# Kernel optimization log

Measured on AMD Instinct MI355X. Metric: run time of the kernel, lower is better.

Reference implementation:

```python
import jax, jax.numpy as jnp
import numpy as np

NUM_CLASSES = 80
NUM_PRIORS = 3
STRIDES = (8, 16, 32)
ANCHORS = (((10, 13), (16, 30), (33, 23)),
           ((30, 61), (62, 45), (59, 119)),
           ((116, 90), (156, 198), (373, 326)))
PRE_TOP_K = 1000
KEEP_TOP_K = 100
IOU_THR = 0.65
SCORE_THR = 0.25
IMG = 640
CLS_OFFSET = 4096.0  # class-offset trick for batched (class-aware) NMS


def _make_priors():
    priors, strides = [], []
    for lvl, s in enumerate(STRIDES):
        fs = IMG // s
        ys, xs = np.meshgrid(np.arange(fs), np.arange(fs), indexing='ij')
        cx = (xs * s).astype(np.float32)[..., None]
        cy = (ys * s).astype(np.float32)[..., None]
        anc = np.asarray(ANCHORS[lvl], np.float32)  # [3,2]
        cx = np.broadcast_to(cx, (fs, fs, NUM_PRIORS))
        cy = np.broadcast_to(cy, (fs, fs, NUM_PRIORS))
        w = np.broadcast_to(anc[None, None, :, 0], (fs, fs, NUM_PRIORS))
        h = np.broadcast_to(anc[None, None, :, 1], (fs, fs, NUM_PRIORS))
        box = np.stack([cx - w / 2, cy - h / 2, cx + w / 2, cy + h / 2], -1).reshape(-1, 4)
        priors.append(box)
        strides.append(np.full((box.shape[0],), s, np.float32))
    return jnp.asarray(np.concatenate(priors)), jnp.asarray(np.concatenate(strides))


def setup_inputs() -> dict:
    key = jax.random.key(0)
    ks = jax.random.split(key, 9)
    shapes = {
        'cls0': (32, 240, 80, 80), 'cls1': (32, 240, 40, 40), 'cls2': (32, 240, 20, 20),
        'bbox0': (32, 12, 80, 80), 'bbox1': (32, 12, 40, 40), 'bbox2': (32, 12, 20, 20),
        'obj0': (32, 3, 80, 80), 'obj1': (32, 3, 40, 40), 'obj2': (32, 3, 20, 20),
    }
    inp = {n: jax.random.normal(k, s, dtype=jnp.float32) for (n, s), k in zip(shapes.items(), ks)}
    priors, strides = _make_priors()
    inp['priors'] = priors
    inp['strides'] = strides
    return inp


def _flatten(x, last):  # [B,C,H,W] -> [B, H*W*priors, last]
    B = x.shape[0]
    return jnp.transpose(x, (0, 2, 3, 1)).reshape(B, -1, last)


def _decode_yolov5(priors, preds, strides):
    # priors [N,4] (x1,y1,x2,y2), preds [B,N,4], strides [N]
    p = jax.nn.sigmoid(preds)
    cx = (priors[:, 0] + priors[:, 2]) * 0.5
    cy = (priors[:, 1] + priors[:, 3]) * 0.5
    w = priors[:, 2] - priors[:, 0]
    h = priors[:, 3] - priors[:, 1]
    xc = (p[..., 0] - 0.5) * 2.0 * strides + cx
    yc = (p[..., 1] - 0.5) * 2.0 * strides + cy
    wp = (p[..., 2] * 2.0) ** 2 * w
    hp = (p[..., 3] * 2.0) ** 2 * h
    return jnp.stack([xc - wp * 0.5, yc - hp * 0.5, xc + wp * 0.5, yc + hp * 0.5], -1)


def _pairwise_iou(b):  # b [K,4]
    area = (b[:, 2] - b[:, 0]) * (b[:, 3] - b[:, 1])
    lt = jnp.maximum(b[:, None, :2], b[None, :, :2])
    rb = jnp.minimum(b[:, None, 2:], b[None, :, 2:])
    wh = jnp.clip(rb - lt, 0.0)
    inter = wh[..., 0] * wh[..., 1]
    return inter / (area[:, None] + area[None, :] - inter + 1e-7)


def _nms_single(boxes, scores):
    # boxes [N,4], scores [N,C]
    flat = scores.reshape(-1)
    top_s, top_i = jax.lax.top_k(flat, PRE_TOP_K)  # sorted desc
    anchor = top_i // NUM_CLASSES
    label = top_i % NUM_CLASSES
    b = boxes[anchor]  # [K,4]
    bo = b + label.astype(boxes.dtype)[:, None] * CLS_OFFSET
    iou = _pairwise_iou(bo)
    valid = top_s > SCORE_THR
    idxs = jnp.arange(PRE_TOP_K)

    def body(i, supp):
        keep_i = jnp.logical_not(supp[i])
        return jnp.where(keep_i & (iou[i] > IOU_THR) & (idxs > i), True, supp)

    supp = jax.lax.fori_loop(0, PRE_TOP_K, body, jnp.logical_not(valid))
    keep = jnp.logical_not(supp) & valid
    k_scores = jnp.where(keep, top_s, 0.0)
    det_s, det_i = jax.lax.top_k(k_scores, KEEP_TOP_K)
    det_b = b[det_i]
    det_l = label[det_i]
    num = jnp.minimum(jnp.sum(keep.astype(jnp.int32)), KEEP_TOP_K)
    return num, det_b, det_s, det_l


def reference(cls0, cls1, cls2, bbox0, bbox1, bbox2, obj0, obj1, obj2, priors, strides):
    cls = jnp.concatenate([_flatten(c, NUM_CLASSES) for c in (cls0, cls1, cls2)], axis=1)
    scores = jax.nn.sigmoid(cls)  # [B,N,C]
    bp = jnp.concatenate([_flatten(b, 4) for b in (bbox0, bbox1, bbox2)], axis=1)
    obj = jnp.concatenate([_flatten(o, 1)[..., 0] for o in (obj0, obj1, obj2)], axis=1)
    scores = scores * jax.nn.sigmoid(obj)[..., None]
    bboxes = _decode_yolov5(priors, bp, strides)  # [B,N,4]
    num, det_b, det_s, det_l = jax.vmap(_nms_single)(bboxes, scores)
    return num, det_b, det_s, det_l
```

## Files before the change

### kernel.cpp

```cpp
#include <hip/hip_runtime.h>
#include <stdint.h>

#define NCLS 80
#define CELLS 8400
#define PRE 1000
#define KEEP 100
#define CAP 4096
#define NBINS 16384
#define NIMG 32
#define SUBS 8
#define SUBCAP 2048
#define GBINS 4096
#define COMPCAP 2048
#define T0 0.75f
#define SCREEN 1.0886f

__device__ __forceinline__ float sigm(float x) { return 1.0f / (1.0f + __expf(-x)); }

__device__ __forceinline__ void lvlinfo(int cell, int& li, int& loc, int& HW) {
  if (cell < 6400)      { li = 0; loc = cell;        HW = 6400; }
  else if (cell < 8000) { li = 1; loc = cell - 6400; HW = 1600; }
  else                  { li = 2; loc = cell - 8000; HW = 400;  }
}

__global__ __launch_bounds__(256) void k_pass1(
    const float* __restrict__ cls0, const float* __restrict__ cls1, const float* __restrict__ cls2,
    const float* __restrict__ obj0, const float* __restrict__ obj1, const float* __restrict__ obj2,
    uint32_t* __restrict__ cnt75, uint64_t* __restrict__ cand75) {
  const int b = blockIdx.y;
  const int bx = blockIdx.x;
  const int sb = bx / 6;
  const int r  = bx - sb * 6;
  const int h  = r & 1;
  const int p  = r >> 1;
  const int c0cell = (sb * 256 + threadIdx.x) * 4;
  if (c0cell >= CELLS) return;
  int li, loc, HW; lvlinfo(c0cell, li, loc, HW);
  const float* cls = li == 0 ? cls0 : (li == 1 ? cls1 : cls2);
  const float* obj = li == 0 ? obj0 : (li == 1 ? obj1 : obj2);

  float4 ov = *(const float4*)(obj + ((size_t)b * 3 + p) * HW + loc);
  float os[4] = { sigm(ov.x), sigm(ov.y), sigm(ov.z), sigm(ov.w) };

  const int sub = bx & (SUBS - 1);
  const float* cp = cls + ((size_t)b * 240 + p * 80 + h * 40) * HW + loc;
  for (int gq = 0; gq < 5; ++gq) {
    float4 v[8];
#pragma unroll
    for (int u = 0; u < 8; ++u)
      v[u] = *(const float4*)(cp + (size_t)(gq * 8 + u) * HW);
#pragma unroll
    for (int u = 0; u < 8; ++u) {
      const int c = h * 40 + gq * 8 + u;
      float vv[4] = { v[u].x, v[u].y, v[u].z, v[u].w };
#pragma unroll
      for (int k = 0; k < 4; ++k) {
        if (vv[k] > SCREEN) {
          float s = sigm(vv[k]) * os[k];
          if (s > T0) {
            uint32_t slot = atomicAdd(&cnt75[b * SUBS + sub], 1u);
            if (slot < SUBCAP) {
              uint32_t flat = (uint32_t)(((c0cell + k) * 3 + p) * 80 + c);
              cand75[((size_t)(b * SUBS + sub)) * SUBCAP + slot] =
                  ((uint64_t)__float_as_uint(s) << 32) | (uint64_t)(0xFFFFFFFFu - flat);
            }
          }
        }
      }
    }
  }
}

__global__ __launch_bounds__(1024) void k_gather(
    const uint64_t* __restrict__ cand75, const uint32_t* __restrict__ cnt75,
    uint32_t* __restrict__ flags,
    const float* __restrict__ bbox0, const float* __restrict__ bbox1, const float* __restrict__ bbox2,
    const float* __restrict__ priors, const float* __restrict__ strides,
    float* __restrict__ topS, int* __restrict__ topLab, float* __restrict__ topBox,
    uint32_t* __restrict__ nvArr) {
  __shared__ uint32_t hist[GBINS];
  __shared__ uint64_t comp[COMPCAP];
  __shared__ uint32_t seg[64];
  __shared__ uint32_t ncomp_s, cb_s;
  const int b = blockIdx.x;
  const int tid = threadIdx.x;
  uint32_t tot = 0; bool bad = false;
  for (int s = 0; s < SUBS; ++s) {
    uint32_t cc = cnt75[b * SUBS + s];
    tot += cc;
    if (cc > SUBCAP) bad = true;
  }
  if (tot < (uint32_t)PRE) bad = true;
  if (bad) { if (tid == 0) flags[b] = 1u; return; }

  for (int i = tid; i < GBINS; i += 1024) hist[i] = 0;
  if (tid == 0) ncomp_s = 0;
  __syncthreads();
  for (int s = 0; s < SUBS; ++s) {
    uint32_t c = cnt75[b * SUBS + s];
    const uint64_t* src = cand75 + ((size_t)(b * SUBS + s)) * SUBCAP;
    for (int i = tid; i < (int)c; i += 1024) {
      uint32_t hi = (uint32_t)(src[i] >> 32);
      uint32_t bin = (hi - 0x3F400000u) >> 10;
      if (bin > GBINS - 1) bin = GBINS - 1;
      atomicAdd(&hist[bin], 1u);
    }
  }
  __syncthreads();
  if (tid < 64) {
    uint32_t s = 0;
    for (int k = 0; k < 64; ++k) s += hist[tid * 64 + k];
    seg[tid] = s;
  }
  __syncthreads();
  if (tid == 0) {
    uint32_t acc = 0; int segi = 0;
    for (int i = 63; i >= 0; --i) {
      if (acc + seg[i] >= (uint32_t)PRE) { segi = i; break; }
      acc += seg[i];
    }
    uint32_t cb = 0;
    for (int k = 63; k >= 0; --k) {
      acc += hist[segi * 64 + k];
      if (acc >= (uint32_t)PRE) { cb = (uint32_t)(segi * 64 + k); break; }
    }
    cb_s = cb;
  }
  __syncthreads();
  const uint32_t cb = cb_s;
  for (int s = 0; s < SUBS; ++s) {
    uint32_t c = cnt75[b * SUBS + s];
    const uint64_t* src = cand75 + ((size_t)(b * SUBS + s)) * SUBCAP;
    for (int i = tid; i < (int)c; i += 1024) {
      uint64_t key = src[i];
      uint32_t hi = (uint32_t)(key >> 32);
      uint32_t bin = (hi - 0x3F400000u) >> 10;
      if (bin > GBINS - 1) bin = GBINS - 1;
      if (bin >= cb) {
        uint32_t pos = atomicAdd(&ncomp_s, 1u);
        if (pos < COMPCAP) comp[pos] = key;
      }
    }
  }
  __syncthreads();
  const uint32_t ncomp = ncomp_s;
  if (ncomp > COMPCAP) { if (tid == 0) flags[b] = 1u; return; }
  const int N = (ncomp <= 1024u) ? 1024 : COMPCAP;
  for (int i = tid; i < N; i += 1024) if (i >= (int)ncomp) comp[i] = 0ull;
  __syncthreads();
  for (int k = 2; k <= N; k <<= 1) {
    for (int j = k >> 1; j > 0; j >>= 1) {
      for (int i = tid; i < N; i += 1024) {
        int p = i ^ j;
        if (p > i) {
          uint64_t a = comp[i], c = comp[p];
          bool asc = (i & k) != 0;
          if (asc ? (a > c) : (a < c)) { comp[i] = c; comp[p] = a; }
        }
      }
      __syncthreads();
    }
  }
  if (tid == 0) nvArr[b] = (uint32_t)PRE;
  for (int t = tid; t < PRE; t += 1024) {
    uint64_t key = comp[t];
    float sc = __uint_as_float((uint32_t)(key >> 32));
    uint32_t flat = 0xFFFFFFFFu - (uint32_t)(key & 0xFFFFFFFFull);
    uint32_t n = flat / 80u; int lab = (int)(flat - n * 80u);
    uint32_t g = n / 3u; uint32_t p = n - g * 3u;
    int li, loc, HW; lvlinfo((int)g, li, loc, HW);
    const float* bb = li == 0 ? bbox0 : (li == 1 ? bbox1 : bbox2);
    size_t o = ((size_t)b * 12 + p * 4) * HW + loc;
    float p0 = sigm(bb[o]);
    float p1 = sigm(bb[o + (size_t)HW]);
    float p2 = sigm(bb[o + 2 * (size_t)HW]);
    float p3 = sigm(bb[o + 3 * (size_t)HW]);
    float4 pr = *(const float4*)(priors + (size_t)n * 4);
    float st = strides[n];
    float cx = (pr.x + pr.z) * 0.5f, cy = (pr.y + pr.w) * 0.5f;
    float w = pr.z - pr.x, hh = pr.w - pr.y;
    float xc = (p0 - 0.5f) * 2.0f * st + cx;
    float yc = (p1 - 0.5f) * 2.0f * st + cy;
    float wp = p2 * 2.0f; wp = wp * wp * w;
    float hp = p3 * 2.0f; hp = hp * hp * hh;
    topS[(size_t)b * PRE + t] = sc;
    topLab[(size_t)b * PRE + t] = lab;
    *(float4*)(topBox + ((size_t)b * PRE + t) * 4) =
        make_float4(xc - wp * 0.5f, yc - hp * 0.5f, xc + wp * 0.5f, yc + hp * 0.5f);
  }
}

__global__ __launch_bounds__(256) void k_zero_hist(uint32_t* __restrict__ hist,
                                                   const uint32_t* __restrict__ flags) {
  __shared__ uint32_t any;
  if (threadIdx.x == 0) {
    uint32_t a = 0;
    for (int i = 0; i < NIMG; ++i) a |= flags[i];
    any = a;
  }
  __syncthreads();
  if (!any) return;
  const int total = NIMG * NBINS;
  for (int i = blockIdx.x * 256 + threadIdx.x; i < total; i += gridDim.x * 256)
    hist[i] = 0;
}

__global__ __launch_bounds__(256) void k_hist_fb(
    const float* __restrict__ cls0, const float* __restrict__ cls1, const float* __restrict__ cls2,
    const float* __restrict__ obj0, const float* __restrict__ obj1, const float* __restrict__ obj2,
    uint32_t* __restrict__ hist, const uint32_t* __restrict__ flags) {
  const int b = blockIdx.y;
  if (flags[b] == 0u) return;
  __shared__ uint32_t h[NBINS];
  for (int i = threadIdx.x; i < NBINS; i += 256) h[i] = 0;
  __syncthreads();
  const int c0 = (blockIdx.x * 256 + threadIdx.x) * 4;
  if (c0 < CELLS) {
    int li, loc, HW; lvlinfo(c0, li, loc, HW);
    const float* cls = li == 0 ? cls0 : (li == 1 ? cls1 : cls2);
    const float* obj = li == 0 ? obj0 : (li == 1 ? obj1 : obj2);
    float os[3][4];
#pragma unroll
    for (int p = 0; p < 3; ++p) {
      float4 o = *(const float4*)(obj + ((size_t)b * 3 + p) * HW + loc);
      os[p][0] = sigm(o.x); os[p][1] = sigm(o.y); os[p][2] = sigm(o.z); os[p][3] = sigm(o.w);
    }
    for (int p = 0; p < 3; ++p) {
      const float* cp = cls + ((size_t)b * 240 + p * 80) * HW + loc;
      for (int c = 0; c < 80; ++c) {
        float4 v = *(const float4*)(cp + (size_t)c * HW);
        float sv[4] = { sigm(v.x) * os[p][0], sigm(v.y) * os[p][1],
                        sigm(v.z) * os[p][2], sigm(v.w) * os[p][3] };
#pragma unroll
        for (int k = 0; k < 4; ++k) {
          if (sv[k] > 0.25f) {
            uint32_t key = (__float_as_uint(sv[k]) - 0x3E800000u) >> 10;
            if (key > NBINS - 1) key = NBINS - 1;
            atomicAdd(&h[key], 1u);
          }
        }
      }
    }
  }
  __syncthreads();
  for (int i = threadIdx.x; i < NBINS; i += 256) {
    uint32_t v = h[i];
    if (v) atomicAdd(&hist[(size_t)b * NBINS + i], v);
  }
}

__global__ __launch_bounds__(256) void k_cutoff_fb(const uint32_t* __restrict__ hist,
                                                   uint32_t* __restrict__ cutoff,
                                                   const uint32_t* __restrict__ flags) {
  const int b = blockIdx.x;
  if (flags[b] == 0u) return;
  __shared__ uint32_t seg[256];
  const uint32_t* hb = hist + (size_t)b * NBINS;
  uint32_t s = 0;
  for (int k = 0; k < 64; ++k) s += hb[threadIdx.x * 64 + k];
  seg[threadIdx.x] = s;
  __syncthreads();
  if (threadIdx.x == 0) {
    uint32_t acc = 0; int segi = -1;
    for (int i = 255; i >= 0; --i) {
      if (acc + seg[i] >= (uint32_t)PRE) { segi = i; break; }
      acc += seg[i];
    }
    uint32_t cut = 0;
    if (segi >= 0) {
      for (int k = 63; k >= 0; --k) {
        acc += hb[segi * 64 + k];
        if (acc >= (uint32_t)PRE) { cut = (uint32_t)(segi * 64 + k); break; }
      }
    }
    cutoff[b] = cut;
  }
}

__global__ __launch_bounds__(256) void k_collect_fb(
    const float* __restrict__ cls0, const float* __restrict__ cls1, const float* __restrict__ cls2,
    const float* __restrict__ obj0, const float* __restrict__ obj1, const float* __restrict__ obj2,
    const uint32_t* __restrict__ cutoff, uint32_t* __restrict__ candCount,
    uint64_t* __restrict__ cand, const uint32_t* __restrict__ flags) {
  const int b = blockIdx.y;
  if (flags[b] == 0u) return;
  const int c0 = (blockIdx.x * 256 + threadIdx.x) * 4;
  if (c0 >= CELLS) return;
  const uint32_t cut = cutoff[b];
  int li, loc, HW; lvlinfo(c0, li, loc, HW);
  const float* cls = li == 0 ? cls0 : (li == 1 ? cls1 : cls2);
  const float* obj = li == 0 ? obj0 : (li == 1 ? obj1 : obj2);
  float os[3][4];
#pragma unroll
  for (int p = 0; p < 3; ++p) {
    float4 o = *(const float4*)(obj + ((size_t)b * 3 + p) * HW + loc);
    os[p][0] = sigm(o.x); os[p][1] = sigm(o.y); os[p][2] = sigm(o.z); os[p][3] = sigm(o.w);
  }
  for (int p = 0; p < 3; ++p) {
    const float* cp = cls + ((size_t)b * 240 + p * 80) * HW + loc;
    for (int c = 0; c < 80; ++c) {
      float4 v = *(const float4*)(cp + (size_t)c * HW);
      float sv[4] = { sigm(v.x) * os[p][0], sigm(v.y) * os[p][1],
                      sigm(v.z) * os[p][2], sigm(v.w) * os[p][3] };
#pragma unroll
      for (int k = 0; k < 4; ++k) {
        float sk = sv[k];
        if (sk > 0.25f) {
          uint32_t key = (__float_as_uint(sk) - 0x3E800000u) >> 10;
          if (key >= cut) {
            uint32_t pos = atomicAdd(&candCount[b], 1u);
            if (pos < CAP) {
              uint32_t flat = (uint32_t)((((c0 + k) * 3 + p) * 80) + c);
              cand[(size_t)b * CAP + pos] =
                  ((uint64_t)__float_as_uint(sk) << 32) | (uint64_t)(0xFFFFFFFFu - flat);
            }
          }
        }
      }
    }
  }
}

__global__ __launch_bounds__(1024) void k_sort_decode_fb(
    const uint64_t* __restrict__ cand, const uint32_t* __restrict__ candCount,
    const float* __restrict__ bbox0, const float* __restrict__ bbox1, const float* __restrict__ bbox2,
    const float* __restrict__ priors, const float* __restrict__ strides,
    float* __restrict__ topS, int* __restrict__ topLab, float* __restrict__ topBox,
    uint32_t* __restrict__ nvArr, const uint32_t* __restrict__ flags) {
  const int b = blockIdx.x;
  if (flags[b] == 0u) return;
  __shared__ uint64_t s[CAP];
  uint32_t cnt = candCount[b]; if (cnt > (uint32_t)CAP) cnt = CAP;
  for (int i = threadIdx.x; i < CAP; i += 1024)
    s[i] = (i < (int)cnt) ? cand[(size_t)b * CAP + i] : 0ull;
  __syncthreads();
  for (int k = 2; k <= CAP; k <<= 1) {
    for (int j = k >> 1; j > 0; j >>= 1) {
      for (int i = threadIdx.x; i < CAP; i += 1024) {
        int p = i ^ j;
        if (p > i) {
          uint64_t a = s[i], c = s[p];
          bool asc = (i & k) != 0;
          if (asc ? (a > c) : (a < c)) { s[i] = c; s[p] = a; }
        }
      }
      __syncthreads();
    }
  }
  const int NV = (int)(cnt < (uint32_t)PRE ? cnt : (uint32_t)PRE);
  if (threadIdx.x == 0) nvArr[b] = (uint32_t)NV;
  for (int t = threadIdx.x; t < PRE; t += 1024) {
    float sc = 0.0f; int lab = 0; float b0 = 0, b1 = 0, b2v = 0, b3 = 0;
    if (t < NV) {
      uint64_t key = s[t];
      sc = __uint_as_float((uint32_t)(key >> 32));
      uint32_t flat = 0xFFFFFFFFu - (uint32_t)(key & 0xFFFFFFFFull);
      uint32_t n = flat / 80u; lab = (int)(flat - n * 80u);
      uint32_t g = n / 3u; uint32_t p = n - g * 3u;
      int li, loc, HW; lvlinfo((int)g, li, loc, HW);
      const float* bb = li == 0 ? bbox0 : (li == 1 ? bbox1 : bbox2);
      size_t o = ((size_t)b * 12 + p * 4) * HW + loc;
      float p0 = sigm(bb[o]);
      float p1 = sigm(bb[o + (size_t)HW]);
      float p2 = sigm(bb[o + 2 * (size_t)HW]);
      float p3 = sigm(bb[o + 3 * (size_t)HW]);
      float4 pr = *(const float4*)(priors + (size_t)n * 4);
      float st = strides[n];
      float cx = (pr.x + pr.z) * 0.5f, cy = (pr.y + pr.w) * 0.5f;
      float w = pr.z - pr.x, hh = pr.w - pr.y;
      float xc = (p0 - 0.5f) * 2.0f * st + cx;
      float yc = (p1 - 0.5f) * 2.0f * st + cy;
      float wp = p2 * 2.0f; wp = wp * wp * w;
      float hp = p3 * 2.0f; hp = hp * hp * hh;
      b0 = xc - wp * 0.5f; b1 = yc - hp * 0.5f; b2v = xc + wp * 0.5f; b3 = yc + hp * 0.5f;
    }
    topS[(size_t)b * PRE + t] = sc;
    topLab[(size_t)b * PRE + t] = lab;
    *(float4*)(topBox + ((size_t)b * PRE + t) * 4) = make_float4(b0, b1, b2v, b3);
  }
}

__global__ __launch_bounds__(256) void k_iou(
    const float* __restrict__ topBox, const int* __restrict__ topLab,
    const uint32_t* __restrict__ nvArr, uint64_t* __restrict__ mask) {
  __shared__ float4 bx[PRE];
  __shared__ int lb[PRE];
  const int b = blockIdx.y;
  const int NV = (int)nvArr[b];
  for (int i = threadIdx.x; i < PRE; i += 256) {
    bx[i] = *(const float4*)(topBox + ((size_t)b * PRE + i) * 4);
    lb[i] = topLab[(size_t)b * PRE + i];
  }
  __syncthreads();
  for (int task = blockIdx.x * 256 + threadIdx.x; task < PRE * 16; task += gridDim.x * 256) {
    const int i = task >> 4, w = task & 15;
    uint64_t m = 0;
    if (i < NV) {
      const float4 a = bx[i]; const int la = lb[i];
      const float areaA = (a.z - a.x) * (a.w - a.y);
      const int j0 = w << 6;
      const int jend = (j0 + 64 < NV) ? j0 + 64 : NV;
      for (int j = (j0 > i + 1 ? j0 : i + 1); j < jend; ++j) {
        if (lb[j] != la) continue;
        const float4 c = bx[j];
        float xx1 = fmaxf(a.x, c.x), yy1 = fmaxf(a.y, c.y);
        float xx2 = fminf(a.z, c.z), yy2 = fminf(a.w, c.w);
        float iw = fmaxf(xx2 - xx1, 0.0f), ih = fmaxf(yy2 - yy1, 0.0f);
        float inter = iw * ih;
        float areaB = (c.z - c.x) * (c.w - c.y);
        float iou = inter / (areaA + areaB - inter + 1e-7f);
        if (iou > 0.65f) m |= (1ull << (j - j0));
      }
    }
    mask[((size_t)b * PRE + i) * 16 + w] = m;
  }
}

__global__ __launch_bounds__(256) void k_scan_out(
    const uint64_t* __restrict__ mask, const float* __restrict__ topS,
    const int* __restrict__ topLab, const float* __restrict__ topBox,
    const uint32_t* __restrict__ nvArr, float* __restrict__ out) {
  __shared__ uint64_t rows[PRE * 16];
  __shared__ uint64_t keepw[16];
  __shared__ uint32_t pref[17];
  const int b = blockIdx.x;
  const int NV = (int)nvArr[b];
  for (int i = threadIdx.x; i < NV * 16; i += 256) rows[i] = mask[(size_t)b * PRE * 16 + i];
  __syncthreads();
  if (threadIdx.x < 64) {
    const int lane = threadIdx.x;
    uint64_t remv = 0, kw = 0;
    for (int w0 = 0; w0 * 64 < NV; ++w0) {
      uint64_t cur = (uint64_t)__shfl((unsigned long long)remv, w0);
      const int ie = (w0 * 64 + 64 < NV) ? w0 * 64 + 64 : NV;
      for (int i = w0 * 64; i < ie; ++i) {
        const int bi = i & 63;
        uint64_t rl = rows[i * 16 + (lane & 15)];
        uint64_t cw = rows[i * 16 + w0];
        const uint64_t keepm = ((cur >> bi) & 1ull) ? 0ull : ~0ull;
        cur |= cw & keepm;
        remv |= rl & keepm;
        kw |= (lane == w0) ? ((1ull << bi) & keepm) : 0ull;
      }
    }
    if (lane < 16) keepw[lane] = kw;
  }
  __syncthreads();
  if (threadIdx.x == 0) {
    uint32_t a = 0;
    for (int w = 0; w < 16; ++w) { pref[w] = a; a += (uint32_t)__popcll((unsigned long long)keepw[w]); }
    pref[16] = a;
  }
  __syncthreads();
  const uint32_t total = pref[16];
  const uint32_t num = total < (uint32_t)KEEP ? total : (uint32_t)KEEP;
  float* o_num = out;
  float* o_box = out + NIMG;
  float* o_s   = out + NIMG + NIMG * KEEP * 4;
  float* o_l   = o_s + NIMG * KEEP;
  if (threadIdx.x == 0) o_num[b] = (float)num;
  const int zstart = NV < KEEP ? NV : KEEP;
  for (int sidx = zstart + threadIdx.x; sidx < KEEP; sidx += 256) {
    ((float4*)o_box)[b * KEEP + sidx] = make_float4(0, 0, 0, 0);
    o_s[b * KEEP + sidx] = 0.0f;
    o_l[b * KEEP + sidx] = 0.0f;
  }
  for (int j = threadIdx.x; j < NV; j += 256) {
    const int wi = j >> 6, bi = j & 63;
    const uint64_t kword = keepw[wi];
    const int isk = (int)((kword >> bi) & 1ull);
    const uint32_t below = pref[wi] + (uint32_t)__popcll((unsigned long long)(kword & ((1ull << bi) - 1ull)));
    const uint32_t slot = isk ? below : (total + (uint32_t)j - below);
    if (slot < (uint32_t)KEEP) {
      ((float4*)o_box)[b * KEEP + slot] = *(const float4*)(topBox + ((size_t)b * PRE + j) * 4);
      o_s[b * KEEP + slot] = isk ? topS[(size_t)b * PRE + j] : 0.0f;
      o_l[b * KEEP + slot] = (float)topLab[(size_t)b * PRE + j];
    }
  }
}

extern "C" void kernel_launch(void* const* d_in, const int* in_sizes, int n_in,
                              void* d_out, int out_size, void* d_ws, size_t ws_size,
                              hipStream_t stream) {
  (void)in_sizes; (void)n_in; (void)out_size; (void)ws_size;
  const float* cls0 = (const float*)d_in[0];
  const float* cls1 = (const float*)d_in[1];
  const float* cls2 = (const float*)d_in[2];
  const float* bbox0 = (const float*)d_in[3];
  const float* bbox1 = (const float*)d_in[4];
  const float* bbox2 = (const float*)d_in[5];
  const float* obj0 = (const float*)d_in[6];
  const float* obj1 = (const float*)d_in[7];
  const float* obj2 = (const float*)d_in[8];
  const float* priors = (const float*)d_in[9];
  const float* strides = (const float*)d_in[10];
  float* out = (float*)d_out;

  char* ws = (char*)d_ws;
  size_t off = 0;
  auto alloc = [&](size_t bytes) -> void* {
    void* p = ws + off;
    off = (off + bytes + 255) & ~(size_t)255;
    return p;
  };
  uint32_t* small     = (uint32_t*)alloc(4096);
  uint32_t* flags     = small;
  uint32_t* cnt75     = small + 32;
  uint32_t* candCount = small + 288;
  uint32_t* cutoff    = small + 320;
  uint32_t* nvArr     = small + 352;
  uint64_t* cand75    = (uint64_t*)alloc((size_t)NIMG * SUBS * SUBCAP * 8);
  uint32_t* hist      = (uint32_t*)alloc((size_t)NIMG * NBINS * 4);
  uint64_t* cand      = (uint64_t*)alloc((size_t)NIMG * CAP * 8);
  float*    topS      = (float*)alloc((size_t)NIMG * PRE * 4);
  int*      topLab    = (int*)alloc((size_t)NIMG * PRE * 4);
  float*    topBox    = (float*)alloc((size_t)NIMG * PRE * 16);
  uint64_t* maskbuf   = (uint64_t*)alloc((size_t)NIMG * PRE * 16 * 8);

  hipMemsetAsync(small, 0, 4096, stream);

  k_pass1<<<dim3(54, NIMG), 256, 0, stream>>>(cls0, cls1, cls2, obj0, obj1, obj2,
                                              cnt75, cand75);
  k_gather<<<NIMG, 1024, 0, stream>>>(cand75, cnt75, flags, bbox0, bbox1, bbox2,
                                      priors, strides, topS, topLab, topBox, nvArr);
  k_zero_hist<<<256, 256, 0, stream>>>(hist, flags);
  dim3 gScan(9, NIMG);
  k_hist_fb<<<gScan, 256, 0, stream>>>(cls0, cls1, cls2, obj0, obj1, obj2, hist, flags);
  k_cutoff_fb<<<NIMG, 256, 0, stream>>>(hist, cutoff, flags);
  k_collect_fb<<<gScan, 256, 0, stream>>>(cls0, cls1, cls2, obj0, obj1, obj2,
                                          cutoff, candCount, cand, flags);
  k_sort_decode_fb<<<NIMG, 1024, 0, stream>>>(cand, candCount, bbox0, bbox1, bbox2,
                                              priors, strides, topS, topLab, topBox, nvArr, flags);
  k_iou<<<dim3(63, NIMG), 256, 0, stream>>>(topBox, topLab, nvArr, maskbuf);
  k_scan_out<<<NIMG, 256, 0, stream>>>(maskbuf, topS, topLab, topBox, nvArr, out);
}
```

Measured before the change: 372.4 us.

## Flatten pass1 into contiguous float4 scan and fuse fallback kernels via last-block

The first pass now walks the class tensor as a flat contiguous float4 stream across many more blocks. It exits early when a block's four vectors are all below the screen threshold and fetches objectness only for surviving values. The fallback path drops the zero-hist, cutoff and sort/decode kernels: histogram zeroing moves into the gather kernel's bail-out path, and cutoff and sort are done by the last-arriving block using atomic counters and fences. This cuts launch count and improves pass1 coalescing and parallelism, but sorting on a 256-thread block is slower and the code relies on fence-based cross-block completion.

```diff
diff --git a/kernel.cpp b/kernel.cpp
--- a/kernel.cpp
+++ b/kernel.cpp
@@ -29,51 +29,61 @@
     uint32_t* __restrict__ cnt75, uint64_t* __restrict__ cand75) {
   const int b = blockIdx.y;
   const int bx = blockIdx.x;
-  const int sb = bx / 6;
-  const int r  = bx - sb * 6;
-  const int h  = r & 1;
-  const int p  = r >> 1;
-  const int c0cell = (sb * 256 + threadIdx.x) * 4;
-  if (c0cell >= CELLS) return;
-  int li, loc, HW; lvlinfo(c0cell, li, loc, HW);
-  const float* cls = li == 0 ? cls0 : (li == 1 ? cls1 : cls2);
-  const float* obj = li == 0 ? obj0 : (li == 1 ? obj1 : obj2);
-
-  float4 ov = *(const float4*)(obj + ((size_t)b * 3 + p) * HW + loc);
-  float os[4] = { sigm(ov.x), sigm(ov.y), sigm(ov.z), sigm(ov.w) };
-
+  int lvl, lb_f4, nf4, HW, cellbase;
+  const float* clsB; const float* objB;
+  if (bx < 375)      { lvl = 0; lb_f4 = bx * 1024;         nf4 = 384000; HW = 6400; cellbase = 0;    clsB = cls0; objB = obj0; }
+  else if (bx < 469) { lvl = 1; lb_f4 = (bx - 375) * 1024; nf4 = 96000;  HW = 1600; cellbase = 6400; clsB = cls1; objB = obj1; }
+  else               { lvl = 2; lb_f4 = (bx - 469) * 1024; nf4 = 24000;  HW = 400;  cellbase = 8000; clsB = cls2; objB = obj2; }
+  const float4* cb4 = (const float4*)(clsB + (size_t)b * 240 * HW);
+  const float* objb = objB + (size_t)b * 3 * HW;
   const int sub = bx & (SUBS - 1);
-  const float* cp = cls + ((size_t)b * 240 + p * 80 + h * 40) * HW + loc;
-  for (int gq = 0; gq < 5; ++gq) {
-    float4 v[8];
+  const int j0 = lb_f4 + threadIdx.x;
+  const int j1 = j0 + 256, j2 = j0 + 512, j3 = j0 + 768;
+
+  float4 v0 = cb4[j0];
+  float4 v1 = cb4[j1 < nf4 ? j1 : j0];
+  float4 v2 = cb4[j2 < nf4 ? j2 : j0];
+  float4 v3 = cb4[j3 < nf4 ? j3 : j0];
+  float m0 = fmaxf(fmaxf(v0.x, v0.y), fmaxf(v0.z, v0.w));
+  float m1 = fmaxf(fmaxf(v1.x, v1.y), fmaxf(v1.z, v1.w));
+  float m2 = fmaxf(fmaxf(v2.x, v2.y), fmaxf(v2.z, v2.w));
+  float m3 = fmaxf(fmaxf(v3.x, v3.y), fmaxf(v3.z, v3.w));
+  if (fmaxf(fmaxf(m0, m1), fmaxf(m2, m3)) <= SCREEN) return;
+
+  auto proc = [&](float4 v, float mv, int j) {
+    if (mv <= SCREEN) return;
+    int ch, w4;
+    if (lvl == 0)      { ch = j / 1600; w4 = j - ch * 1600; }
+    else if (lvl == 1) { ch = j / 400;  w4 = j - ch * 400; }
+    else               { ch = j / 100;  w4 = j - ch * 100; }
+    const int p = ch / 80;
+    const int c = ch - p * 80;
+    float vv[4] = { v.x, v.y, v.z, v.w };
 #pragma unroll
-    for (int u = 0; u < 8; ++u)
-      v[u] = *(const float4*)(cp + (size_t)(gq * 8 + u) * HW);
-#pragma unroll
-    for (int u = 0; u < 8; ++u) {
-      const int c = h * 40 + gq * 8 + u;
-      float vv[4] = { v[u].x, v[u].y, v[u].z, v[u].w };
-#pragma unroll
-      for (int k = 0; k < 4; ++k) {
-        if (vv[k] > SCREEN) {
-          float s = sigm(vv[k]) * os[k];
-          if (s > T0) {
-            uint32_t slot = atomicAdd(&cnt75[b * SUBS + sub], 1u);
-            if (slot < SUBCAP) {
-              uint32_t flat = (uint32_t)(((c0cell + k) * 3 + p) * 80 + c);
-              cand75[((size_t)(b * SUBS + sub)) * SUBCAP + slot] =
-                  ((uint64_t)__float_as_uint(s) << 32) | (uint64_t)(0xFFFFFFFFu - flat);
-            }
+    for (int k = 0; k < 4; ++k) {
+      if (vv[k] > SCREEN) {
+        float ov = objb[p * HW + w4 * 4 + k];
+        float s = sigm(vv[k]) * sigm(ov);
+        if (s > T0) {
+          uint32_t slot = atomicAdd(&cnt75[b * SUBS + sub], 1u);
+          if (slot < SUBCAP) {
+            uint32_t flat = (uint32_t)(((cellbase + w4 * 4 + k) * 3 + p) * 80 + c);
+            cand75[((size_t)(b * SUBS + sub)) * SUBCAP + slot] =
+                ((uint64_t)__float_as_uint(s) << 32) | (uint64_t)(0xFFFFFFFFu - flat);
           }
         }
       }
     }
-  }
+  };
+  proc(v0, m0, j0);
+  if (j1 < nf4) proc(v1, m1, j1);
+  if (j2 < nf4) proc(v2, m2, j2);
+  if (j3 < nf4) proc(v3, m3, j3);
 }
 
 __global__ __launch_bounds__(1024) void k_gather(
     const uint64_t* __restrict__ cand75, const uint32_t* __restrict__ cnt75,
-    uint32_t* __restrict__ flags,
+    uint32_t* __restrict__ flags, uint32_t* __restrict__ histg,
     const float* __restrict__ bbox0, const float* __restrict__ bbox1, const float* __restrict__ bbox2,
     const float* __restrict__ priors, const float* __restrict__ strides,
     float* __restrict__ topS, int* __restrict__ topLab, float* __restrict__ topBox,
@@ -91,7 +101,11 @@
     if (cc > SUBCAP) bad = true;
   }
   if (tot < (uint32_t)PRE) bad = true;
-  if (bad) { if (tid == 0) flags[b] = 1u; return; }
+  if (bad) {
+    if (tid == 0) flags[b] = 1u;
+    for (int i = tid; i < NBINS; i += 1024) histg[(size_t)b * NBINS + i] = 0;
+    return;
+  }
 
   for (int i = tid; i < GBINS; i += 1024) hist[i] = 0;
   if (tid == 0) ncomp_s = 0;
@@ -144,7 +158,11 @@
   }
   __syncthreads();
   const uint32_t ncomp = ncomp_s;
-  if (ncomp > COMPCAP) { if (tid == 0) flags[b] = 1u; return; }
+  if (ncomp > COMPCAP) {
+    if (tid == 0) flags[b] = 1u;
+    for (int i = tid; i < NBINS; i += 1024) histg[(size_t)b * NBINS + i] = 0;
+    return;
+  }
   const int N = (ncomp <= 1024u) ? 1024 : COMPCAP;
   for (int i = tid; i < N; i += 1024) if (i >= (int)ncomp) comp[i] = 0ull;
   __syncthreads();
@@ -190,28 +208,16 @@
   }
 }
 
-__global__ __launch_bounds__(256) void k_zero_hist(uint32_t* __restrict__ hist,
-                                                   const uint32_t* __restrict__ flags) {
-  __shared__ uint32_t any;
-  if (threadIdx.x == 0) {
-    uint32_t a = 0;
-    for (int i = 0; i < NIMG; ++i) a |= flags[i];
-    any = a;
-  }
-  __syncthreads();
-  if (!any) return;
-  const int total = NIMG * NBINS;
-  for (int i = blockIdx.x * 256 + threadIdx.x; i < total; i += gridDim.x * 256)
-    hist[i] = 0;
-}
-
 __global__ __launch_bounds__(256) void k_hist_fb(
     const float* __restrict__ cls0, const float* __restrict__ cls1, const float* __restrict__ cls2,
     const float* __restrict__ obj0, const float* __restrict__ obj1, const float* __restrict__ obj2,
-    uint32_t* __restrict__ hist, const uint32_t* __restrict__ flags) {
+    uint32_t* __restrict__ hist, const uint32_t* __restrict__ flags,
+    uint32_t* __restrict__ histDone, uint32_t* __restrict__ cutoff) {
   const int b = blockIdx.y;
   if (flags[b] == 0u) return;
   __shared__ uint32_t h[NBINS];
+  __shared__ uint32_t seg[256];
+  __shared__ uint32_t lastArrive;
   for (int i = threadIdx.x; i < NBINS; i += 256) h[i] = 0;
   __syncthreads();
   const int c0 = (blockIdx.x * 256 + threadIdx.x) * 4;
@@ -247,17 +253,15 @@
     uint32_t v = h[i];
     if (v) atomicAdd(&hist[(size_t)b * NBINS + i], v);
   }
-}
-
-__global__ __launch_bounds__(256) void k_cutoff_fb(const uint32_t* __restrict__ hist,
-                                                   uint32_t* __restrict__ cutoff,
-                                                   const uint32_t* __restrict__ flags) {
-  const int b = blockIdx.x;
-  if (flags[b] == 0u) return;
-  __shared__ uint32_t seg[256];
-  const uint32_t* hb = hist + (size_t)b * NBINS;
+  __syncthreads();
+  __threadfence();
+  if (threadIdx.x == 0) lastArrive = atomicAdd(&histDone[b], 1u);
+  __syncthreads();
+  if (lastArrive != 8) return;
+  __threadfence();
+  uint32_t* hb = hist + (size_t)b * NBINS;
   uint32_t s = 0;
-  for (int k = 0; k < 64; ++k) s += hb[threadIdx.x * 64 + k];
+  for (int k = 0; k < 64; ++k) s += atomicOr(&hb[threadIdx.x * 64 + k], 0u);
   seg[threadIdx.x] = s;
   __syncthreads();
   if (threadIdx.x == 0) {
@@ -269,7 +273,7 @@
     uint32_t cut = 0;
     if (segi >= 0) {
       for (int k = 63; k >= 0; --k) {
-        acc += hb[segi * 64 + k];
+        acc += atomicOr(&hb[segi * 64 + k], 0u);
         if (acc >= (uint32_t)PRE) { cut = (uint32_t)(segi * 64 + k); break; }
       }
     }
@@ -281,62 +285,65 @@
     const float* __restrict__ cls0, const float* __restrict__ cls1, const float* __restrict__ cls2,
     const float* __restrict__ obj0, const float* __restrict__ obj1, const float* __restrict__ obj2,
     const uint32_t* __restrict__ cutoff, uint32_t* __restrict__ candCount,
-    uint64_t* __restrict__ cand, const uint32_t* __restrict__ flags) {
+    uint64_t* __restrict__ cand, const uint32_t* __restrict__ flags,
+    uint32_t* __restrict__ collectDone,
+    const float* __restrict__ bbox0, const float* __restrict__ bbox1, const float* __restrict__ bbox2,
+    const float* __restrict__ priors, const float* __restrict__ strides,
+    float* __restrict__ topS, int* __restrict__ topLab, float* __restrict__ topBox,
+    uint32_t* __restrict__ nvArr) {
   const int b = blockIdx.y;
   if (flags[b] == 0u) return;
+  __shared__ uint64_t s[CAP];
+  __shared__ uint32_t lastArrive;
+  const uint32_t cut = cutoff[b];
   const int c0 = (blockIdx.x * 256 + threadIdx.x) * 4;
-  if (c0 >= CELLS) return;
-  const uint32_t cut = cutoff[b];
-  int li, loc, HW; lvlinfo(c0, li, loc, HW);
-  const float* cls = li == 0 ? cls0 : (li == 1 ? cls1 : cls2);
-  const float* obj = li == 0 ? obj0 : (li == 1 ? obj1 : obj2);
-  float os[3][4];
+  if (c0 < CELLS) {
+    int li, loc, HW; lvlinfo(c0, li, loc, HW);
+    const float* cls = li == 0 ? cls0 : (li == 1 ? cls1 : cls2);
+    const float* obj = li == 0 ? obj0 : (li == 1 ? obj1 : obj2);
+    float os[3][4];
 #pragma unroll
-  for (int p = 0; p < 3; ++p) {
-    float4 o = *(const float4*)(obj + ((size_t)b * 3 + p) * HW + loc);
-    os[p][0] = sigm(o.x); os[p][1] = sigm(o.y); os[p][2] = sigm(o.z); os[p][3] = sigm(o.w);
-  }
-  for (int p = 0; p < 3; ++p) {
-    const float* cp = cls + ((size_t)b * 240 + p * 80) * HW + loc;
-    for (int c = 0; c < 80; ++c) {
-      float4 v = *(const float4*)(cp + (size_t)c * HW);
-      float sv[4] = { sigm(v.x) * os[p][0], sigm(v.y) * os[p][1],
-                      sigm(v.z) * os[p][2], sigm(v.w) * os[p][3] };
+    for (int p = 0; p < 3; ++p) {
+      float4 o = *(const float4*)(obj + ((size_t)b * 3 + p) * HW + loc);
+      os[p][0] = sigm(o.x); os[p][1] = sigm(o.y); os[p][2] = sigm(o.z); os[p][3] = sigm(o.w);
+    }
+    for (int p = 0; p < 3; ++p) {
+      const float* cp = cls + ((size_t)b * 240 + p * 80) * HW + loc;
+      for (int c = 0; c < 80; ++c) {
+        float4 v = *(const float4*)(cp + (size_t)c * HW);
+        float sv[4] = { sigm(v.x) * os[p][0], sigm(v.y) * os[p][1],
+                        sigm(v.z) * os[p][2], sigm(v.w) * os[p][3] };
 #pragma unroll
-      for (int k = 0; k < 4; ++k) {
-        float sk = sv[k];
-        if (sk > 0.25f) {
-          uint32_t key = (__float_as_uint(sk) - 0x3E800000u) >> 10;
-          if (key >= cut) {
-            uint32_t pos = atomicAdd(&candCount[b], 1u);
-            if (pos < CAP) {
-              uint32_t flat = (uint32_t)((((c0 + k) * 3 + p) * 80) + c);
-              cand[(size_t)b * CAP + pos] =
-                  ((uint64_t)__float_as_uint(sk) << 32) | (uint64_t)(0xFFFFFFFFu - flat);
+        for (int k = 0; k < 4; ++k) {
+          float sk = sv[k];
+          if (sk > 0.25f) {
+            uint32_t key = (__float_as_uint(sk) - 0x3E800000u) >> 10;
+            if (key >= cut) {
+              uint32_t pos = atomicAdd(&candCount[b], 1u);
+              if (pos < CAP) {
+                uint32_t flat = (uint32_t)((((c0 + k) * 3 + p) * 80) + c);
+                cand[(size_t)b * CAP + pos] =
+                    ((uint64_t)__float_as_uint(sk) << 32) | (uint64_t)(0xFFFFFFFFu - flat);
+              }
             }
           }
         }
       }
     }
   }
-}
-
-__global__ __launch_bounds__(1024) void k_sort_decode_fb(
-    const uint64_t* __restrict__ cand, const uint32_t* __restrict__ candCount,
-    const float* __restrict__ bbox0, const float* __restrict__ bbox1, const float* __restrict__ bbox2,
-    const float* __restrict__ priors, const float* __restrict__ strides,
-    float* __restrict__ topS, int* __restrict__ topLab, float* __restrict__ topBox,
-    uint32_t* __restrict__ nvArr, const uint32_t* __restrict__ flags) {
-  const int b = blockIdx.x;
-  if (flags[b] == 0u) return;
-  __shared__ uint64_t s[CAP];
-  uint32_t cnt = candCount[b]; if (cnt > (uint32_t)CAP) cnt = CAP;
-  for (int i = threadIdx.x; i < CAP; i += 1024)
+  __syncthreads();
+  __threadfence();
+  if (threadIdx.x == 0) lastArrive = atomicAdd(&collectDone[b], 1u);
+  __syncthreads();
+  if (lastArrive != 8) return;
+  __threadfence();
+  uint32_t cnt = atomicOr(&candCount[b], 0u); if (cnt > (uint32_t)CAP) cnt = CAP;
+  for (int i = threadIdx.x; i < CAP; i += 256)
     s[i] = (i < (int)cnt) ? cand[(size_t)b * CAP + i] : 0ull;
   __syncthreads();
   for (int k = 2; k <= CAP; k <<= 1) {
     for (int j = k >> 1; j > 0; j >>= 1) {
-      for (int i = threadIdx.x; i < CAP; i += 1024) {
+      for (int i = threadIdx.x; i < CAP; i += 256) {
         int p = i ^ j;
         if (p > i) {
           uint64_t a = s[i], c = s[p];
@@ -349,7 +356,7 @@
   }
   const int NV = (int)(cnt < (uint32_t)PRE ? cnt : (uint32_t)PRE);
   if (threadIdx.x == 0) nvArr[b] = (uint32_t)NV;
-  for (int t = threadIdx.x; t < PRE; t += 1024) {
+  for (int t = threadIdx.x; t < PRE; t += 256) {
     float sc = 0.0f; int lab = 0; float b0 = 0, b1 = 0, b2v = 0, b3 = 0;
     if (t < NV) {
       uint64_t key = s[t];
@@ -503,12 +510,14 @@
     off = (off + bytes + 255) & ~(size_t)255;
     return p;
   };
-  uint32_t* small     = (uint32_t*)alloc(4096);
-  uint32_t* flags     = small;
-  uint32_t* cnt75     = small + 32;
-  uint32_t* candCount = small + 288;
-  uint32_t* cutoff    = small + 320;
-  uint32_t* nvArr     = small + 352;
+  uint32_t* small       = (uint32_t*)alloc(4096);
+  uint32_t* flags       = small;
+  uint32_t* cnt75       = small + 32;
+  uint32_t* candCount   = small + 288;
+  uint32_t* cutoff      = small + 320;
+  uint32_t* nvArr       = small + 352;
+  uint32_t* histDone    = small + 384;
+  uint32_t* collectDone = small + 416;
   uint64_t* cand75    = (uint64_t*)alloc((size_t)NIMG * SUBS * SUBCAP * 8);
   uint32_t* hist      = (uint32_t*)alloc((size_t)NIMG * NBINS * 4);
   uint64_t* cand      = (uint64_t*)alloc((size_t)NIMG * CAP * 8);
@@ -519,18 +528,17 @@
 
   hipMemsetAsync(small, 0, 4096, stream);
 
-  k_pass1<<<dim3(54, NIMG), 256, 0, stream>>>(cls0, cls1, cls2, obj0, obj1, obj2,
-                                              cnt75, cand75);
-  k_gather<<<NIMG, 1024, 0, stream>>>(cand75, cnt75, flags, bbox0, bbox1, bbox2,
+  k_pass1<<<dim3(493, NIMG), 256, 0, stream>>>(cls0, cls1, cls2, obj0, obj1, obj2,
+                                               cnt75, cand75);
+  k_gather<<<NIMG, 1024, 0, stream>>>(cand75, cnt75, flags, hist, bbox0, bbox1, bbox2,
                                       priors, strides, topS, topLab, topBox, nvArr);
-  k_zero_hist<<<256, 256, 0, stream>>>(hist, flags);
   dim3 gScan(9, NIMG);
-  k_hist_fb<<<gScan, 256, 0, stream>>>(cls0, cls1, cls2, obj0, obj1, obj2, hist, flags);
-  k_cutoff_fb<<<NIMG, 256, 0, stream>>>(hist, cutoff, flags);
+  k_hist_fb<<<gScan, 256, 0, stream>>>(cls0, cls1, cls2, obj0, obj1, obj2, hist, flags,
+                                       histDone, cutoff);
   k_collect_fb<<<gScan, 256, 0, stream>>>(cls0, cls1, cls2, obj0, obj1, obj2,
-                                          cutoff, candCount, cand, flags);
-  k_sort_decode_fb<<<NIMG, 1024, 0, stream>>>(cand, candCount, bbox0, bbox1, bbox2,
-                                              priors, strides, topS, topLab, topBox, nvArr, flags);
+                                          cutoff, candCount, cand, flags, collectDone,
+                                          bbox0, bbox1, bbox2, priors, strides,
+                                          topS, topLab, topBox, nvArr);
   k_iou<<<dim3(63, NIMG), 256, 0, stream>>>(topBox, topLab, nvArr, maskbuf);
   k_scan_out<<<NIMG, 256, 0, stream>>>(maskbuf, topS, topLab, topBox, nvArr, out);
 }
```

Result: slower. 861.4 us (+131.3%).
